# Kernel optimization log

Measured on AMD Instinct MI355X. Metric: run time of the kernel, lower is better.

## Reference

```python
import jax, jax.numpy as jnp
import numpy as np

VOCAB = 32
UTT_LEN = 16
NUM_MEANING_TYPES = 5
MEANINGS_PER_TYPE = 10
SUPPORT_SIZE = 100000  # = MEANINGS_PER_TYPE ** NUM_MEANING_TYPES
BATCH = 2048


def setup_inputs() -> dict:
    key = jax.random.key(0)
    k1, k2, k3 = jax.random.split(key, 3)
    # query utterances: [utt_len, batch] token ids
    utts = jax.random.randint(k1, (UTT_LEN, BATCH), 0, VOCAB, dtype=jnp.int64)
    # support set is stored as one-hot encoded utterances [S, utt_len*vocab]
    support_tokens = jax.random.randint(k2, (SUPPORT_SIZE, UTT_LEN), 0, VOCAB)
    support = jax.nn.one_hot(support_tokens, VOCAB, dtype=jnp.float32)
    support = support.reshape(SUPPORT_SIZE, UTT_LEN * VOCAB)
    # meanings table [S, num_meaning_types]
    meanings_t = jax.random.randint(k3, (SUPPORT_SIZE, NUM_MEANING_TYPES), 0,
                                    MEANINGS_PER_TYPE, dtype=jnp.int64)
    return {"utts": utts, "support": support, "meanings_t": meanings_t}


def reference(utts, support, meanings_t):
    # utts: [M, N] ints; support: [S, M*V] floats; meanings_t: [S, T] ints
    M, N = utts.shape
    # one-hot encode queries: [N, M, V] -> [N, M*V]
    batch_fluffy = jax.nn.one_hot(utts.T, VOCAB, dtype=jnp.float32).reshape(N, M * VOCAB)
    batch_sq = jnp.sum(batch_fluffy * batch_fluffy, axis=1)        # [N]
    support_sq = jnp.sum(support * support, axis=1)                # [S]
    cross = batch_fluffy @ support.T                                # [N, S]
    squared_dist = batch_sq[:, None] + support_sq[None, :] - 2.0 * cross
    # top-1 smallest distance (K=1)
    top1 = jnp.argmin(squared_dist, axis=1)                         # [N]
    meanings = meanings_t[top1]                                     # [N, T]
    return jax.nn.one_hot(meanings, MEANINGS_PER_TYPE, dtype=jnp.float32)
```

## Files before the change

kernel.cpp:

```cpp
#include <hip/hip_runtime.h>
#include <stdint.h>

#define S_ROWS 100000
#define NQ     2048
#define M_POS  16
#define VOCABS 32
#define WPB    8
#define GROUPS 8
#define CHUNKS 125
#define RC     800
#define KITER  25
#define KPAD   264

__global__ __launch_bounds__(256) void knn_decode(const float* __restrict__ support,
                                                  uint8_t* __restrict__ tok) {
    int wave = (blockIdx.x * 256 + threadIdx.x) >> 6;
    int lane = threadIdx.x & 63;
    if (wave >= S_ROWS) return;
    const float4* rowp = (const float4*)(support + (size_t)wave * 512) + lane * 2;
    float4 f0 = rowp[0];
    float4 f1 = rowp[1];
    float base = (float)((lane & 3) * 64);
    float v = f0.x * (base + 0.f)  + f0.y * (base + 8.f)  + f0.z * (base + 16.f) + f0.w * (base + 24.f)
            + f1.x * (base + 32.f) + f1.y * (base + 40.f) + f1.z * (base + 48.f) + f1.w * (base + 56.f);
    v += __shfl_xor(v, 1);
    v += __shfl_xor(v, 2);
    if ((lane & 3) == 0) {
        int p = lane >> 2;
        tok[(size_t)wave * 16 + p] = (uint8_t)(v + 0.5f);
    }
}

__device__ __forceinline__ void FA(uint32_t a, uint32_t b, uint32_t c,
                                   uint32_t& s, uint32_t& co) {
    uint32_t x = a ^ b;
    s  = x ^ c;
    co = (a & b) | (x & c);
}
__device__ __forceinline__ void HA(uint32_t a, uint32_t b, uint32_t& s, uint32_t& co) {
    s = a ^ b; co = a & b;
}

__global__ __launch_bounds__(256, 4) void knn_score(const int* __restrict__ utts,
                                                    const uint8_t* __restrict__ tok,
                                                    uint32_t* __restrict__ partial) {
    __shared__ uint32_t smem[32 * KPAD];
    uint32_t* table = smem;
    uint32_t* keys  = smem;

    const int bid = blockIdx.x;
    const int g   = bid & 7;
    const int c   = bid >> 3;
    const int t   = threadIdx.x;

    #pragma unroll
    for (int i = 0; i < 16; ++i) table[t + 256 * i] = 0u;
    __syncthreads();

    {
        int q = g * 256 + t;
        int wb = t >> 5, j = t & 31;
        #pragma unroll
        for (int m = 0; m < M_POS; ++m) {
            int v = utts[m * NQ + q];
            atomicOr(&table[(m * VOCABS + v) * WPB + wb], 1u << j);
        }
    }
    __syncthreads();

    const int w   = t & 7;
    const int sub = t >> 3;
    const int r0  = c * RC;
    const uint32_t* tw = table + w;

    uint32_t cp0=0,cp1=0,cp2=0,cp3=0,cp4=0;
    uint32_t k0p=0,k1p=0,k2p=0,k3p=0,k4p=0;

    const uint4* tbase = (const uint4*)(tok + (size_t)(r0 + sub) * 16);

    #pragma unroll
    for (int k = 0; k < KITER; ++k) {
        uint4 ta = tbase[32 * k];
        uint32_t b[16];
        b[0]  = tw[ (ta.x        & 0xFFu) +  0*256];
        b[1]  = tw[((ta.x >> 8)  & 0xFFu) +  1*256];
        b[2]  = tw[((ta.x >> 16) & 0xFFu) +  2*256];
        b[3]  = tw[((ta.x >> 24)        ) +  3*256];
        b[4]  = tw[ (ta.y        & 0xFFu) +  4*256];
        b[5]  = tw[((ta.y >> 8)  & 0xFFu) +  5*256];
        b[6]  = tw[((ta.y >> 16) & 0xFFu) +  6*256];
        b[7]  = tw[((ta.y >> 24)        ) +  7*256];
        b[8]  = tw[ (ta.z        & 0xFFu) +  8*256];
        b[9]  = tw[((ta.z >> 8)  & 0xFFu) +  9*256];
        b[10] = tw[((ta.z >> 16) & 0xFFu) + 10*256];
        b[11] = tw[((ta.z >> 24)        ) + 11*256];
        b[12] = tw[ (ta.w        & 0xFFu) + 12*256];
        b[13] = tw[((ta.w >> 8)  & 0xFFu) + 13*256];
        b[14] = tw[((ta.w >> 16) & 0xFFu) + 14*256];
        b[15] = tw[((ta.w >> 24)        ) + 15*256];

        uint32_t s10,s11,s12,s13,s14, c10,c11,c12,c13,c14;
        FA(b[0],b[1],b[2],   s10,c10);
        FA(b[3],b[4],b[5],   s11,c11);
        FA(b[6],b[7],b[8],   s12,c12);
        FA(b[9],b[10],b[11], s13,c13);
        FA(b[12],b[13],b[14],s14,c14);
        uint32_t s2a,c2a,s2b,c2b;
        FA(s10,s11,s12, s2a,c2a);
        FA(s13,s14,b[15], s2b,c2b);
        uint32_t n0,h0;  HA(s2a,s2b, n0,h0);
        uint32_t u,cu,vv,cv,x2,cx,n1,cy;
        FA(c10,c11,c12, u,cu);
        FA(c13,c14,c2a, vv,cv);
        FA(u,vv,c2b,    x2,cx);
        HA(x2,h0,       n1,cy);
        uint32_t y4,cz,n2,cw,n3,n4;
        FA(cu,cv,cx, y4,cz);
        HA(y4,cy,    n2,cw);
        HA(cz,cw,    n3,n4);

        uint32_t eq = ~(n4 ^ cp4);
        uint32_t gt = n4 & ~cp4;
        gt |= eq & (n3 & ~cp3);  eq &= ~(n3 ^ cp3);
        gt |= eq & (n2 & ~cp2);  eq &= ~(n2 ^ cp2);
        gt |= eq & (n1 & ~cp1);  eq &= ~(n1 ^ cp1);
        gt |= eq & (n0 & ~cp0);

        uint32_t ng = ~gt;
        cp0 = (gt & n0) | (ng & cp0);
        cp1 = (gt & n1) | (ng & cp1);
        cp2 = (gt & n2) | (ng & cp2);
        cp3 = (gt & n3) | (ng & cp3);
        cp4 = (gt & n4) | (ng & cp4);
        k0p = ( k       & 1) ? (k0p & ng) | gt : (k0p & ng);
        k1p = ((k >> 1) & 1) ? (k1p & ng) | gt : (k1p & ng);
        k2p = ((k >> 2) & 1) ? (k2p & ng) | gt : (k2p & ng);
        k3p = ((k >> 3) & 1) ? (k3p & ng) | gt : (k3p & ng);
        k4p = ((k >> 4) & 1) ? (k4p & ng) | gt : (k4p & ng);
    }

    __syncthreads();

    {
        uint32_t C = 0x1FFFFu - (uint32_t)(r0 + sub);
        #pragma unroll
        for (int j = 0; j < 32; ++j) {
            uint32_t cnt = ((cp0>>j)&1u) | (((cp1>>j)&1u)<<1) | (((cp2>>j)&1u)<<2)
                         | (((cp3>>j)&1u)<<3) | (((cp4>>j)&1u)<<4);
            uint32_t kk  = ((k0p>>j)&1u) | (((k1p>>j)&1u)<<1) | (((k2p>>j)&1u)<<2)
                         | (((k3p>>j)&1u)<<3) | (((k4p>>j)&1u)<<4);
            uint32_t key = (cnt << 17) + C - (kk << 5);
            keys[j * KPAD + t] = key;
        }
    }
    __syncthreads();

    {
        int w2 = t & 7, j2 = t >> 3;
        const uint32_t* kp = keys + j2 * KPAD + w2;
        uint32_t best = 0;
        #pragma unroll
        for (int i = 0; i < 32; ++i) {
            uint32_t v = kp[8 * i];
            best = best > v ? best : v;
        }
        partial[(size_t)c * NQ + g * 256 + w2 * 32 + j2] = best;
    }
}

__global__ __launch_bounds__(256) void knn_reduce_out(const uint32_t* __restrict__ partial,
                                                      const int* __restrict__ meanings,
                                                      float* __restrict__ out) {
    int q = blockIdx.x * 256 + threadIdx.x;
    if (q >= NQ) return;
    uint32_t best = 0;
    #pragma unroll 5
    for (int c = 0; c < CHUNKS; ++c) {
        uint32_t v = partial[(size_t)c * NQ + q];
        best = best > v ? best : v;
    }
    int idx = 0x1FFFF - (int)(best & 0x1FFFFu);
    float* o = out + (size_t)q * 50;
    #pragma unroll
    for (int tt = 0; tt < 5; ++tt) {
        int mv = meanings[(size_t)idx * 5 + tt];
        #pragma unroll
        for (int mm = 0; mm < 10; ++mm) o[tt * 10 + mm] = (mm == mv) ? 1.0f : 0.0f;
    }
}

extern "C" void kernel_launch(void* const* d_in, const int* in_sizes, int n_in,
                              void* d_out, int out_size, void* d_ws, size_t ws_size,
                              hipStream_t stream) {
    const int*   utts     = (const int*)d_in[0];
    const float* support  = (const float*)d_in[1];
    const int*   meanings = (const int*)d_in[2];
    float* out = (float*)d_out;

    uint8_t*  tok     = (uint8_t*)d_ws;
    uint32_t* partial = (uint32_t*)((char*)d_ws + (size_t)S_ROWS * 16);

    knn_decode<<<(S_ROWS + 3) / 4, 256, 0, stream>>>(support, tok);
    knn_score<<<GROUPS * CHUNKS, 256, 0, stream>>>(utts, tok, partial);
    knn_reduce_out<<<NQ / 256, 256, 0, stream>>>(partial, meanings, out);
}
```

Baseline: 325.8 us.

## Replace partial-result buffer and reduction with global atomicMax into per-query best

Each score block now merges its per-query best key straight into a global array with atomicMax, instead of writing a chunk-by-query partial buffer that the final kernel reduced over 125 chunks. The best array is zeroed inside the decode kernel, and the output kernel reads one value per query. The scoring loop goes from full unrolling to unroll 5, and the position-bit update becomes a branchless mask form. This drops the partial-buffer traffic and the serial reduction, at the cost of contended global atomics and possibly less ILP in the main loop.

Result: faster. 313.0 us, median of 2 (-3.9%).

```diff
diff --git a/kernel.cpp b/kernel.cpp
--- a/kernel.cpp
+++ b/kernel.cpp
@@ -13,7 +13,9 @@
 #define KPAD   264
 
 __global__ __launch_bounds__(256) void knn_decode(const float* __restrict__ support,
-                                                  uint8_t* __restrict__ tok) {
+                                                  uint8_t* __restrict__ tok,
+                                                  uint32_t* __restrict__ best) {
+    if (blockIdx.x < 8) best[blockIdx.x * 256 + threadIdx.x] = 0u;
     int wave = (blockIdx.x * 256 + threadIdx.x) >> 6;
     int lane = threadIdx.x & 63;
     if (wave >= S_ROWS) return;
@@ -43,7 +45,7 @@
 
 __global__ __launch_bounds__(256, 4) void knn_score(const int* __restrict__ utts,
                                                     const uint8_t* __restrict__ tok,
-                                                    uint32_t* __restrict__ partial) {
+                                                    uint32_t* __restrict__ best) {
     __shared__ uint32_t smem[32 * KPAD];
     uint32_t* table = smem;
     uint32_t* keys  = smem;
@@ -78,7 +80,7 @@
 
     const uint4* tbase = (const uint4*)(tok + (size_t)(r0 + sub) * 16);
 
-    #pragma unroll
+    #pragma unroll 5
     for (int k = 0; k < KITER; ++k) {
         uint4 ta = tbase[32 * k];
         uint32_t b[16];
@@ -132,11 +134,16 @@
         cp2 = (gt & n2) | (ng & cp2);
         cp3 = (gt & n3) | (ng & cp3);
         cp4 = (gt & n4) | (ng & cp4);
-        k0p = ( k       & 1) ? (k0p & ng) | gt : (k0p & ng);
-        k1p = ((k >> 1) & 1) ? (k1p & ng) | gt : (k1p & ng);
-        k2p = ((k >> 2) & 1) ? (k2p & ng) | gt : (k2p & ng);
-        k3p = ((k >> 3) & 1) ? (k3p & ng) | gt : (k3p & ng);
-        k4p = ((k >> 4) & 1) ? (k4p & ng) | gt : (k4p & ng);
+        uint32_t kb0 = 0u - (uint32_t)( k        & 1);
+        uint32_t kb1 = 0u - (uint32_t)((k >> 1)  & 1);
+        uint32_t kb2 = 0u - (uint32_t)((k >> 2)  & 1);
+        uint32_t kb3 = 0u - (uint32_t)((k >> 3)  & 1);
+        uint32_t kb4 = 0u - (uint32_t)((k >> 4)  & 1);
+        k0p = (k0p & ng) | (gt & kb0);
+        k1p = (k1p & ng) | (gt & kb1);
+        k2p = (k2p & ng) | (gt & kb2);
+        k3p = (k3p & ng) | (gt & kb3);
+        k4p = (k4p & ng) | (gt & kb4);
     }
 
     __syncthreads();
@@ -158,28 +165,23 @@
     {
         int w2 = t & 7, j2 = t >> 3;
         const uint32_t* kp = keys + j2 * KPAD + w2;
-        uint32_t best = 0;
+        uint32_t bestv = 0;
         #pragma unroll
         for (int i = 0; i < 32; ++i) {
             uint32_t v = kp[8 * i];
-            best = best > v ? best : v;
+            bestv = bestv > v ? bestv : v;
         }
-        partial[(size_t)c * NQ + g * 256 + w2 * 32 + j2] = best;
-    }
-}
-
-__global__ __launch_bounds__(256) void knn_reduce_out(const uint32_t* __restrict__ partial,
-                                                      const int* __restrict__ meanings,
-                                                      float* __restrict__ out) {
+        atomicMax(&best[g * 256 + w2 * 32 + j2], bestv);
+    }
+}
+
+__global__ __launch_bounds__(256) void knn_out(const uint32_t* __restrict__ best,
+                                               const int* __restrict__ meanings,
+                                               float* __restrict__ out) {
     int q = blockIdx.x * 256 + threadIdx.x;
     if (q >= NQ) return;
-    uint32_t best = 0;
-    #pragma unroll 5
-    for (int c = 0; c < CHUNKS; ++c) {
-        uint32_t v = partial[(size_t)c * NQ + q];
-        best = best > v ? best : v;
-    }
-    int idx = 0x1FFFF - (int)(best & 0x1FFFFu);
+    uint32_t b = best[q];
+    int idx = 0x1FFFF - (int)(b & 0x1FFFFu);
     float* o = out + (size_t)q * 50;
     #pragma unroll
     for (int tt = 0; tt < 5; ++tt) {
@@ -197,10 +199,10 @@
     const int*   meanings = (const int*)d_in[2];
     float* out = (float*)d_out;
 
-    uint8_t*  tok     = (uint8_t*)d_ws;
-    uint32_t* partial = (uint32_t*)((char*)d_ws + (size_t)S_ROWS * 16);
-
-    knn_decode<<<(S_ROWS + 3) / 4, 256, 0, stream>>>(support, tok);
-    knn_score<<<GROUPS * CHUNKS, 256, 0, stream>>>(utts, tok, partial);
-    knn_reduce_out<<<NQ / 256, 256, 0, stream>>>(partial, meanings, out);
-}
+    uint8_t*  tok  = (uint8_t*)d_ws;
+    uint32_t* best = (uint32_t*)((char*)d_ws + (size_t)S_ROWS * 16);
+
+    knn_decode<<<(S_ROWS + 3) / 4, 256, 0, stream>>>(support, tok, best);
+    knn_score<<<GROUPS * CHUNKS, 256, 0, stream>>>(utts, tok, best);
+    knn_out<<<NQ / 256, 256, 0, stream>>>(best, meanings, out);
+}
```
